# Optimization experiments

Measured on AMD Instinct MI355X. Metric: run time of the kernel, lower is better.

The kernel has to match this reference:

```python
import jax, jax.numpy as jnp
import numpy as np

BLANK = 1   # Offsets.GO
NEG = -1e30  # effective -inf that stays finite under logaddexp


def setup_inputs() -> dict:
    key = jax.random.key(0)
    k1, k2, k3, k4 = jax.random.split(key, 4)
    T, B, V, S = 1000, 64, 512, 100
    logits = jax.random.normal(k1, (T, B, V), dtype=jnp.float32)
    log_prob = jax.nn.log_softmax(logits, axis=-1)  # ctc_loss expects log-probs
    input_lengths = jax.random.randint(k2, (B,), T // 2, T + 1, dtype=jnp.int32)
    # target tokens avoid PAD(0)/GO(1,blank)/EOS(2), matching the masked_select semantics
    targets = jax.random.randint(k3, (B, S), 3, V, dtype=jnp.int32)
    target_lengths = jax.random.randint(k4, (B,), S // 2, S + 1, dtype=jnp.int32)
    return {"log_prob": log_prob, "input_lengths": input_lengths,
            "targets": targets, "target_lengths": target_lengths}


def _ctc_loss_sum(log_prob, input_lengths, targets, target_lengths):
    # log_prob: (T, B, V) log-softmax outputs; targets: (B, S) padded labels
    T, B, V = log_prob.shape
    S = targets.shape[1]
    Se = 2 * S + 1  # extended label sequence: blank-interleaved

    ext = jnp.full((B, Se), BLANK, dtype=targets.dtype).at[:, 1::2].set(targets)
    pos = jnp.arange(Se)
    ext_len = 2 * target_lengths + 1                      # (B,)
    valid = pos[None, :] < ext_len[:, None]               # (B, Se)
    ext_m2 = jnp.pad(ext[:, :-2], ((0, 0), (2, 0)), constant_values=BLANK)
    allow_skip = (ext != BLANK) & (ext != ext_m2) & (pos[None, :] >= 2)

    # emit[t, b, s] = log_prob[t, b, ext[b, s]]  -> (T, B, Se)
    emit = jnp.take_along_axis(log_prob, jnp.broadcast_to(ext[None], (T, B, Se)), axis=2)

    # alpha init at t=0
    alpha = jnp.full((B, Se), NEG, dtype=log_prob.dtype)
    alpha = alpha.at[:, 0].set(emit[0, :, 0])
    alpha = alpha.at[:, 1].set(jnp.where(target_lengths > 0, emit[0, :, 1], NEG))
    alpha = jnp.where(valid, alpha, NEG)

    def step(alpha, xt):
        emit_t, t = xt
        a1 = alpha
        a2 = jnp.pad(alpha[:, :-1], ((0, 0), (1, 0)), constant_values=NEG)
        a3 = jnp.where(allow_skip,
                       jnp.pad(alpha[:, :-2], ((0, 0), (2, 0)), constant_values=NEG),
                       NEG)
        new = jnp.logaddexp(jnp.logaddexp(a1, a2), a3) + emit_t
        new = jnp.where(valid, new, NEG)
        # freeze alpha once past each sample's input length
        alpha = jnp.where((t < input_lengths)[:, None], new, alpha)
        return alpha, None

    alpha, _ = jax.lax.scan(step, alpha, (emit[1:], jnp.arange(1, T)))

    last = 2 * target_lengths  # index of trailing blank in extended sequence
    a_last = jnp.take_along_axis(alpha, last[:, None], axis=1)[:, 0]
    a_prev = jnp.take_along_axis(alpha, jnp.maximum(last - 1, 0)[:, None], axis=1)[:, 0]
    loglik = jnp.logaddexp(a_last, a_prev)
    loss = -loglik
    # zero_infinity=True: infeasible alignments contribute 0
    loss = jnp.where(loglik < 0.5 * NEG, 0.0, loss)
    return jnp.sum(loss)  # reduction='sum'


def reference(log_prob, input_lengths, targets, target_lengths):
    return _ctc_loss_sum(log_prob, input_lengths, targets, target_lengths)
```

## Files before the change

### kernel.cpp

```cpp
#include <hip/hip_runtime.h>


#define NEGF (-1e30f)

constexpr int CT_T  = 1000;
constexpr int CT_B  = 64;
constexpr int CT_V  = 512;
constexpr int CT_S  = 100;
constexpr int CT_Se = 201;
constexpr int RT    = 15;
constexpr float LOG2E = 1.4426950408889634f;
constexpr float LN2   = 0.6931471805599453f;
constexpr float SHIFT = 5.0f;

typedef float f4 __attribute__((ext_vector_type(4)));

#if __has_builtin(__builtin_amdgcn_exp2f) && __has_builtin(__builtin_amdgcn_logf)
__device__ __forceinline__ float fexp2(float x) { return __builtin_amdgcn_exp2f(x); }
__device__ __forceinline__ float flog2(float x) { return __builtin_amdgcn_logf(x); }
__device__ __forceinline__ float frcp(float x)  { return __builtin_amdgcn_rcpf(x); }
#else
__device__ __forceinline__ float fexp2(float x) { return exp2f(x); }
__device__ __forceinline__ float flog2(float x) { return log2f(x); }
__device__ __forceinline__ float frcp(float x)  { return 1.0f / x; }
#endif

__device__ __forceinline__ float lae2_b2(float x, float y) {
    float m = fmaxf(x, y);
    float d = fminf(x, y) - m;
    return m + flog2(1.0f + fexp2(d));
}
__device__ __forceinline__ float lae3_b2(float x, float y, float z) {
    float m = fmaxf(fmaxf(x, y), z);
    float s = fexp2(x - m) + fexp2(y - m) + fexp2(z - m);
    return m + flog2(s);
}

__device__ __forceinline__ float wave_shr1(float x) {
    return __int_as_float(__builtin_amdgcn_update_dpp(
        0, __float_as_int(x), 0x138, 0xf, 0xf, true));
}
__device__ __forceinline__ float wave_max_nonneg(float x) {
#define DPPMAX(ctrl) x = fmaxf(x, __int_as_float(__builtin_amdgcn_update_dpp( \
        0, __float_as_int(x), ctrl, 0xf, 0xf, true)))
    DPPMAX(0x111); DPPMAX(0x112); DPPMAX(0x114); DPPMAX(0x118);
    DPPMAX(0x142); DPPMAX(0x143);
#undef DPPMAX
    return __int_as_float(__builtin_amdgcn_readlane(__float_as_int(x), 63));
}

typedef const __attribute__((address_space(1))) unsigned int* as1_uint_ptr;
typedef __attribute__((address_space(3))) unsigned int* as3_uint_ptr;
__device__ __forceinline__ void gld16(const void* g, void* l) {
    __builtin_amdgcn_global_load_lds((as1_uint_ptr)g, (as3_uint_ptr)l, 16, 0, 0);
}

#define WAIT_VM0() do { \
    asm volatile("s_waitcnt vmcnt(0)" ::: "memory"); \
    __builtin_amdgcn_sched_barrier(0); } while (0)
#define DRAIN_LGKM() asm volatile("s_waitcnt lgkmcnt(0)" ::: "memory")

__global__ __launch_bounds__(256, 1) void ctc_alpha_pp(
    const float* __restrict__ logp,
    const int*   __restrict__ in_len,
    const int*   __restrict__ tgt,
    const int*   __restrict__ tgt_len,
    float*       __restrict__ loss_ws)
{
    __shared__ __align__(16) float stage[2][RT][CT_V];
    __shared__ __align__(16) float hand[260];

    const int b    = blockIdx.x;
    const int tid  = threadIdx.x;
    const int wv   = tid >> 6;
    const int lane = tid & 63;
    const int Tin  = in_len[b];
    const int Lt   = tgt_len[b];
    const int lim  = 2 * Lt + 1;
    const int* tg  = tgt + b * CT_S;

    const int NT = (Tin - 1 + RT - 1) / RT;

    const int s0 = 4 * lane, s1 = s0 + 1, s3 = s0 + 3;
    const int i1 = min((s1 - 1) >> 1, CT_S - 1);
    const int i3 = min((s3 - 1) >> 1, CT_S - 1);
    const int c1 = tg[i1];
    const int c3 = tg[i3];
    const float sk1 = ((s1 >= 3) && (s1 < CT_Se) && (c1 != tg[max(i1 - 1, 0)])) ? 1.f : 0.f;
    const float sk3 = ((s3 >= 3) && (s3 < CT_Se) && (c3 != tg[max(i3 - 1, 0)])) ? 1.f : 0.f;
    const float m0 = (s0     < lim) ? 1.f : 0.f;
    const float m2 = (s0 + 2 < lim) ? 1.f : 0.f;
    const float Sy = (s0 + 1 < lim) ? SHIFT : -1000.f;
    const float Sw = (s0 + 3 < lim) ? SHIFT : -1000.f;

    float a0 = 0.f, a1 = 0.f, a2 = 0.f, a3 = 0.f, pa3 = 0.f;
    if (tid == 0) {
        const float* r0 = logp + (size_t)b * CT_V;
        a0 = fexp2(fmaf(r0[1], LOG2E, SHIFT));
        if (Lt > 0) a1 = fexp2(fmaf(r0[c1], LOG2E, SHIFT));
    }
    float rs = 0.f;

    float ex[RT], ey[RT], ez[RT], ew[RT];

    const int rb = (wv == 3) ? 8 : 0;
    const int re = (wv == 3) ? RT : 8;

    auto issue = [&](int c) {
        const int tb = 1 + RT * c;
        const int buf = c & 1;
        for (int r = rb; r < re; ++r) {
            const int t = min(tb + r, CT_T - 1);
            const char* g = (const char*)(logp + ((size_t)t * CT_B + b) * CT_V)
                          + (size_t)lane * 16;
            gld16(g,        &stage[buf][r][0]);
            gld16(g + 1024, &stage[buf][r][256]);
        }
    };

    auto prep = [&](int tn) {
        const int buf = tn & 1;
        #pragma unroll
        for (int s = 0; s < RT; ++s) {
            float gb = stage[buf][s][1];
            float g1 = stage[buf][s][c1];
            float g3 = stage[buf][s][c3];
            float eb = fexp2(fmaf(gb, LOG2E, SHIFT));
            ey[s] = fexp2(fmaf(g1, LOG2E, Sy));
            ew[s] = fexp2(fmaf(g3, LOG2E, Sw));
            ex[s] = eb * m0;
            ez[s] = eb * m2;
        }
    };

    auto renorm = [&]() {
        float lm = wave_max_nonneg(fmaxf(fmaxf(a0, a1), fmaxf(a2, a3)));
        if (lm > 0.f) {
            float sc = frcp(lm);
            rs += flog2(lm);
            a0 *= sc; a1 *= sc; a2 *= sc; a3 *= sc;
            pa3 = wave_shr1(a3);
        }
    };

    auto recurse = [&](int i) {
        if (i > 0) {
            f4 h = *reinterpret_cast<f4*>(&hand[4 * lane]);
            a0 = h.x; a1 = h.y; a2 = h.z; a3 = h.w;
            rs = hand[256];
            pa3 = wave_shr1(a3);
        }
        const int tb = 1 + RT * i;
        const bool guard = (tb + RT > Tin);
        #pragma unroll
        for (int s = 0; s < RT; ++s) {
            float n0 = (a0 + pa3) * ex[s];
            float n1 = fmaf(sk1, pa3, a1 + a0) * ey[s];
            float n2 = (a2 + a1) * ez[s];
            float n3 = fmaf(sk3, a1, a3 + a2) * ew[s];
            if (!guard || (tb + s < Tin)) { a0 = n0; a1 = n1; a2 = n2; a3 = n3; }
            pa3 = wave_shr1(a3);
        }
        renorm();
        f4 h; h.x = a0; h.y = a1; h.z = a2; h.w = a3;
        *reinterpret_cast<f4*>(&hand[4 * lane]) = h;
        if (lane == 0) hand[256] = rs;
        DRAIN_LGKM();
    };

    if (wv >= 2) {
        WAIT_VM0();
        issue(0); issue(1);
        WAIT_VM0();
    }
    __builtin_amdgcn_s_barrier();
    if (wv == 0) prep(0);
    __builtin_amdgcn_s_barrier();

    for (int i = 0; i < NT; ++i) {
        if (wv < 2) {
            if ((i & 1) == wv)   recurse(i);
            else if (i + 1 < NT) prep(i + 1);
        } else {
            if (i + 2 < NT) issue(i + 2);
            WAIT_VM0();
        }
        __builtin_amdgcn_s_barrier();
    }

    if (wv >= 2) return;
    if (wv != ((NT - 1) & 1)) return;

    const int last = 2 * Lt;
    const int prev = max(last - 1, 0);
    const int lr = last & 3, lidx = last >> 2;
    float av = (lr == 0) ? a0 : (lr == 1) ? a1 : (lr == 2) ? a2 : a3;
    float a_last = __shfl(av, lidx);
    const int pr = prev & 3, pidx = prev >> 2;
    float pv = (pr == 0) ? a0 : (pr == 1) ? a1 : (pr == 2) ? a2 : a3;
    float a_prev = __shfl(pv, pidx);

    float sum = a_last + a_prev;
    float loss = 0.f;
    if (sum > 0.f)
        loss = -(flog2(sum) + rs - SHIFT * (float)Tin) * LN2;
    if (lane == 0) loss_ws[b] = loss;
}

__global__ __launch_bounds__(64) void ctc_alpha_fb(
    const float* __restrict__ logp, const int* __restrict__ in_len,
    const int* __restrict__ tgt, const int* __restrict__ tgt_len,
    float* __restrict__ loss_ws)
{
    const int b = blockIdx.x, lane = threadIdx.x;
    const int Tin = in_len[b], Lt = tgt_len[b];
    const int ext_len = 2 * Lt + 1;
    const int* tg = tgt + b * CT_S;
    const int s0 = 4 * lane, s1 = s0 + 1, s3 = s0 + 3;
    const int i1 = min((s1 - 1) >> 1, CT_S - 1);
    const int i3 = min((s3 - 1) >> 1, CT_S - 1);
    const int c1 = tg[i1], c3 = tg[i3];
    const bool skip1 = (s1 >= 3) && (s1 < CT_Se) && (c1 != tg[max(i1 - 1, 0)]);
    const bool skip3 = (s3 >= 3) && (s3 < CT_Se) && (c3 != tg[max(i3 - 1, 0)]);
    const bool v0 = s0 < ext_len, v1 = s1 < ext_len;
    const bool v2 = (s0 + 2) < ext_len, v3 = s3 < ext_len;
    const float* row0 = logp + (long long)b * CT_V;
    const long long stride = (long long)CT_B * CT_V;
    float a0 = NEGF, a1 = NEGF, a2 = NEGF, a3 = NEGF;
    if (lane == 0) {
        a0 = row0[1] * LOG2E;
        if (ext_len > 1) a1 = row0[c1] * LOG2E;
    }
    float3 E0, E1, E2, E3;
    auto ld = [&](float3& e, int t) {
        int tt = min(t, CT_T - 1);
        const float* r = row0 + (long long)tt * stride;
        e.x = r[1] * LOG2E; e.y = r[c1] * LOG2E; e.z = r[c3] * LOG2E;
    };
    auto step = [&](const float3& e) {
        float pa3 = __shfl_up(a3, 1);
        if (lane == 0) pa3 = NEGF;
        float z1 = skip1 ? pa3 : NEGF;
        float z3 = skip3 ? a1 : NEGF;
        float n0 = v0 ? lae2_b2(a0, pa3)    + e.x : NEGF;
        float n1 = v1 ? lae3_b2(a1, a0, z1) + e.y : NEGF;
        float n2 = v2 ? lae2_b2(a2, a1)     + e.x : NEGF;
        float n3 = v3 ? lae3_b2(a3, a2, z3) + e.z : NEGF;
        a0 = n0; a1 = n1; a2 = n2; a3 = n3;
    };
    ld(E0, 1); ld(E1, 2); ld(E2, 3); ld(E3, 4);
    for (int t = 1; t < Tin; t += 4) {
        step(E0); ld(E0, t + 4);
        if (t + 1 < Tin) { step(E1); ld(E1, t + 5); }
        if (t + 2 < Tin) { step(E2); ld(E2, t + 6); }
        if (t + 3 < Tin) { step(E3); ld(E3, t + 7); }
    }
    const int last = 2 * Lt, prev = max(last - 1, 0);
    const int lr = last & 3, lidx = last >> 2;
    float av = (lr == 0) ? a0 : (lr == 1) ? a1 : (lr == 2) ? a2 : a3;
    float a_last = __shfl(av, lidx);
    const int pr = prev & 3, pidx = prev >> 2;
    float pv = (pr == 0) ? a0 : (pr == 1) ? a1 : (pr == 2) ? a2 : a3;
    float a_prev = __shfl(pv, pidx);
    float loglik = lae2_b2(a_last, a_prev) * LN2;
    float loss = (loglik < 0.5f * NEGF) ? 0.0f : -loglik;
    if (lane == 0) loss_ws[b] = loss;
}

__global__ __launch_bounds__(64) void ctc_sum(const float* __restrict__ loss_ws,
                                              float* __restrict__ out)
{
    float v = loss_ws[threadIdx.x];
    #pragma unroll
    for (int o = 32; o > 0; o >>= 1) v += __shfl_down(v, o);
    if (threadIdx.x == 0) out[0] = v;
}

extern "C" void kernel_launch(void* const* d_in, const int* in_sizes, int n_in,
                              void* d_out, int out_size, void* d_ws, size_t ws_size,
                              hipStream_t stream) {
    const float* logp    = (const float*)d_in[0];
    const int*   in_len  = (const int*)d_in[1];
    const int*   tgt     = (const int*)d_in[2];
    const int*   tgt_len = (const int*)d_in[3];
    float* out = (float*)d_out;
    float* loss_ws = (float*)d_ws;

    if (ws_size >= 256 * sizeof(float)) {
        hipLaunchKernelGGL(ctc_alpha_pp, dim3(CT_B), dim3(256), 0, stream,
                           logp, in_len, tgt, tgt_len, loss_ws);
    } else {
        hipLaunchKernelGGL(ctc_alpha_fb, dim3(CT_B), dim3(64), 0, stream,
                           logp, in_len, tgt, tgt_len, loss_ws);
    }
    hipLaunchKernelGGL(ctc_sum, dim3(1), dim3(64), 0, stream, loss_ws, out);
}
```

Before: 225.1 us.

## Gather only needed logit columns into LDS with triple-buffered counted waits

Rather than staging full 512-wide logit rows into LDS, each loader wave now issues per-lane 4-byte global-to-LDS gathers of just the target-label columns and the blank column. A third buffer and a fifth wave are added so loads run three chunks ahead, and the waits use counted vmcnt instead of draining to zero. This is meant to cut wasted bandwidth and LDS traffic and to hide more latency, at the cost of many more small scattered load instructions and a more fragile wait-count scheme.

```diff
diff --git a/kernel.cpp b/kernel.cpp
--- a/kernel.cpp
+++ b/kernel.cpp
@@ -51,23 +51,26 @@
 
 typedef const __attribute__((address_space(1))) unsigned int* as1_uint_ptr;
 typedef __attribute__((address_space(3))) unsigned int* as3_uint_ptr;
-__device__ __forceinline__ void gld16(const void* g, void* l) {
-    __builtin_amdgcn_global_load_lds((as1_uint_ptr)g, (as3_uint_ptr)l, 16, 0, 0);
-}
-
-#define WAIT_VM0() do { \
-    asm volatile("s_waitcnt vmcnt(0)" ::: "memory"); \
+__device__ __forceinline__ void gld4(const void* g, void* l) {
+    __builtin_amdgcn_global_load_lds((as1_uint_ptr)g, (as3_uint_ptr)l, 4, 0, 0);
+}
+
+#define WAIT_VM(n) do { \
+    asm volatile("s_waitcnt vmcnt(" #n ")" ::: "memory"); \
     __builtin_amdgcn_sched_barrier(0); } while (0)
+#define WAIT_VM0() WAIT_VM(0)
 #define DRAIN_LGKM() asm volatile("s_waitcnt lgkmcnt(0)" ::: "memory")
 
-__global__ __launch_bounds__(256, 1) void ctc_alpha_pp(
+__global__ __launch_bounds__(320, 1) void ctc_alpha_pp(
     const float* __restrict__ logp,
     const int*   __restrict__ in_len,
     const int*   __restrict__ tgt,
     const int*   __restrict__ tgt_len,
     float*       __restrict__ loss_ws)
 {
-    __shared__ __align__(16) float stage[2][RT][CT_V];
+    __shared__ __align__(16) float sc1[3][RT][64];
+    __shared__ __align__(16) float sc3[3][RT][64];
+    __shared__ __align__(16) float sbl[3][64];
     __shared__ __align__(16) float hand[260];
 
     const int b    = blockIdx.x;
@@ -103,28 +106,50 @@
 
     float ex[RT], ey[RT], ez[RT], ew[RT];
 
-    const int rb = (wv == 3) ? 8 : 0;
-    const int re = (wv == 3) ? RT : 8;
-
     auto issue = [&](int c) {
-        const int tb = 1 + RT * c;
-        const int buf = c & 1;
-        for (int r = rb; r < re; ++r) {
-            const int t = min(tb + r, CT_T - 1);
-            const char* g = (const char*)(logp + ((size_t)t * CT_B + b) * CT_V)
-                          + (size_t)lane * 16;
-            gld16(g,        &stage[buf][r][0]);
-            gld16(g + 1024, &stage[buf][r][256]);
-        }
+        const int q = c % 3, tb = 1 + RT * c;
+        if (wv == 2) {
+            #pragma unroll
+            for (int r = 0; r < 10; ++r) {
+                const int t = min(tb + r, CT_T - 1);
+                const float* rp = logp + ((size_t)t * CT_B + b) * CT_V;
+                gld4(rp + c1, &sc1[q][r][0]);
+            }
+        } else if (wv == 3) {
+            #pragma unroll
+            for (int r = 0; r < 10; ++r) {
+                const int t = min(tb + r, CT_T - 1);
+                const float* rp = logp + ((size_t)t * CT_B + b) * CT_V;
+                gld4(rp + c3, &sc3[q][r][0]);
+            }
+        } else {
+            #pragma unroll
+            for (int r = 10; r < RT; ++r) {
+                const int t = min(tb + r, CT_T - 1);
+                const float* rp = logp + ((size_t)t * CT_B + b) * CT_V;
+                gld4(rp + c1, &sc1[q][r][0]);
+            }
+            #pragma unroll
+            for (int r = 10; r < RT; ++r) {
+                const int t = min(tb + r, CT_T - 1);
+                const float* rp = logp + ((size_t)t * CT_B + b) * CT_V;
+                gld4(rp + c3, &sc3[q][r][0]);
+            }
+            const int tl = min(tb + min(lane, RT - 1), CT_T - 1);
+            gld4(logp + ((size_t)tl * CT_B + b) * CT_V + 1, &sbl[q][0]);
+        }
+    };
+    auto gate_counted = [&]() {
+        if (wv == 4) { WAIT_VM(11); } else { WAIT_VM(10); }
     };
 
     auto prep = [&](int tn) {
-        const int buf = tn & 1;
+        const int q = tn % 3;
         #pragma unroll
         for (int s = 0; s < RT; ++s) {
-            float gb = stage[buf][s][1];
-            float g1 = stage[buf][s][c1];
-            float g3 = stage[buf][s][c3];
+            float gb = sbl[q][s];
+            float g1 = sc1[q][s][lane];
+            float g3 = sc3[q][s][lane];
             float eb = fexp2(fmaf(gb, LOG2E, SHIFT));
             ey[s] = fexp2(fmaf(g1, LOG2E, Sy));
             ew[s] = fexp2(fmaf(g3, LOG2E, Sw));
@@ -170,8 +195,8 @@
 
     if (wv >= 2) {
         WAIT_VM0();
-        issue(0); issue(1);
-        WAIT_VM0();
+        issue(0); issue(1); issue(2);
+        gate_counted();
     }
     __builtin_amdgcn_s_barrier();
     if (wv == 0) prep(0);
@@ -182,8 +207,12 @@
             if ((i & 1) == wv)   recurse(i);
             else if (i + 1 < NT) prep(i + 1);
         } else {
-            if (i + 2 < NT) issue(i + 2);
-            WAIT_VM0();
+            if (i + 3 < NT) {
+                issue(i + 3);
+                gate_counted();
+            } else if (i + 2 < NT) {
+                WAIT_VM0();
+            }
         }
         __builtin_amdgcn_s_barrier();
     }
@@ -287,7 +316,7 @@
     float* loss_ws = (float*)d_ws;
 
     if (ws_size >= 256 * sizeof(float)) {
-        hipLaunchKernelGGL(ctc_alpha_pp, dim3(CT_B), dim3(256), 0, stream,
+        hipLaunchKernelGGL(ctc_alpha_pp, dim3(CT_B), dim3(320), 0, stream,
                            logp, in_len, tgt, tgt_len, loss_ws);
     } else {
         hipLaunchKernelGGL(ctc_alpha_fb, dim3(CT_B), dim3(64), 0, stream,
```

After: 211.1 us. 1.07x faster.
